# Kernel tuning notes

Hardware: AMD Instinct MI355X
Metric: run time of the kernel (lower is better)

Reference implementation:

```python
import jax, jax.numpy as jnp
import numpy as np

D_MODEL = 1024
NUM_HEADS = 16
D_K = D_MODEL // NUM_HEADS
ROPE_THETA = 10000.0


def setup_inputs() -> dict:
    key = jax.random.key(0)
    kx, kq, kk, kv, ko = jax.random.split(key, 5)
    B, S = 4, 2048
    std = (2.0 / (D_MODEL + D_MODEL)) ** 0.5
    def w(k):
        return jax.random.truncated_normal(k, -3.0, 3.0, (D_MODEL, D_MODEL), jnp.float32) * std
    return {
        "x": jax.random.normal(kx, (B, S, D_MODEL), jnp.float32),
        "Wq": w(kq), "Wk": w(kk), "Wv": w(kv), "Wo": w(ko),
    }


def _apply_rope(t):
    # t: [B, H, S, d_k]
    S, dk = t.shape[-2], t.shape[-1]
    inv_freq = 1.0 / (ROPE_THETA ** (jnp.arange(0, dk, 2) / dk))  # [dk/2]
    angles = jnp.outer(jnp.arange(S), inv_freq)                    # [S, dk/2]
    cos = jnp.repeat(jnp.cos(angles), 2, axis=-1).astype(t.dtype)  # [S, dk]
    sin = jnp.repeat(jnp.sin(angles), 2, axis=-1).astype(t.dtype)
    t_even = t[..., 0::2]
    t_odd = t[..., 1::2]
    t_rot = jnp.stack([-t_odd, t_even], axis=-1).reshape(t.shape)
    return t * cos + t_rot * sin


def reference(x, Wq, Wk, Wv, Wo):
    B, S, D = x.shape
    H, dk = NUM_HEADS, D_K
    q = jnp.einsum("bsi,io->bso", x, Wq).reshape(B, S, H, dk).swapaxes(1, 2)
    k = jnp.einsum("bsi,io->bso", x, Wk).reshape(B, S, H, dk).swapaxes(1, 2)
    v = jnp.einsum("bsi,io->bso", x, Wv).reshape(B, S, H, dk).swapaxes(1, 2)
    q = _apply_rope(q)
    k = _apply_rope(k)
    scores = jnp.einsum("bhqd,bhkd->bhqk", q, k) / (dk ** 0.5)  # [B,H,S,S]
    causal = jnp.tril(jnp.ones((S, S), dtype=bool))
    scores = jnp.where(causal, scores, -jnp.inf)
    attn = jax.nn.softmax(scores, axis=-1)
    out = jnp.einsum("bhqk,bhkd->bhqd", attn, v)  # [B,H,S,dk]
    out = out.swapaxes(1, 2).reshape(B, S, D)
    return jnp.einsum("bsi,io->bso", out, Wo)
```

## Files before the change

### kernel.cpp

```cpp
#include <hip/hip_runtime.h>
#include <hip/hip_bf16.h>

#define SEQ   2048
#define NB    4
#define NH    16
#define DK    64
#define DM    1024
#define MROWS (NB * SEQ)
#define WEL   (DM * DM)

typedef __bf16 bf16_t;
typedef __bf16 bf16x8 __attribute__((ext_vector_type(8)));
typedef __bf16 bf16x4 __attribute__((ext_vector_type(4)));
typedef float  f32x4  __attribute__((ext_vector_type(4)));

#define MFMA16(a, b, c) __builtin_amdgcn_mfma_f32_16x16x32_bf16((a), (b), (c), 0, 0, 0)

__device__ __forceinline__ void gl2lds16(const bf16_t* g, bf16_t* l) {
    __builtin_amdgcn_global_load_lds(
        (const __attribute__((address_space(1))) unsigned int*)g,
        (__attribute__((address_space(3))) unsigned int*)l, 16, 0, 0);
}

#define BAR()   __builtin_amdgcn_s_barrier()
#define SCB()   __builtin_amdgcn_sched_barrier(0)
#define LGK0()  asm volatile("s_waitcnt lgkmcnt(0)")
#define LGK8()  asm volatile("s_waitcnt lgkmcnt(8)")
#define VMC(N)  asm volatile("s_waitcnt vmcnt(" #N ")")

__global__ __launch_bounds__(256) void prep_kernel(
    const float* __restrict__ x,
    const float* __restrict__ Wq, const float* __restrict__ Wk,
    const float* __restrict__ Wv, const float* __restrict__ Wo,
    bf16_t* __restrict__ xb, bf16_t* __restrict__ Wqkvt,
    bf16_t* __restrict__ Wot, float2* __restrict__ rope)
{
    __shared__ float T[32][33];
    const int bid = blockIdx.x;
    const int tid = threadIdx.x;

    if (bid < 8192) {
        const int i = (bid * 256 + tid) * 4;
        const float4 v = *(const float4*)(x + i);
        bf16x4 o;
        o[0] = (bf16_t)v.x; o[1] = (bf16_t)v.y;
        o[2] = (bf16_t)v.z; o[3] = (bf16_t)v.w;
        *(bf16x4*)(xb + i) = o;
    } else if (bid < 12288) {
        const int wb = bid - 8192;
        const int w  = wb >> 10;
        const int b10 = wb & 1023;
        const float* W = (w == 0) ? Wq : (w == 1) ? Wk : (w == 2) ? Wv : Wo;
        bf16_t* Wt = (w == 3) ? Wot : Wqkvt + (size_t)w * WEL;
        const int tk0 = (b10 >> 5) << 5;
        const int tn0 = (b10 & 31) << 5;
        const int r = tid >> 5, c = tid & 31;
#pragma unroll
        for (int i = 0; i < 4; ++i)
            T[r + i * 8][c] = W[(size_t)(tk0 + r + i * 8) * DM + tn0 + c];
        __syncthreads();
#pragma unroll
        for (int i = 0; i < 4; ++i)
            Wt[(size_t)(tn0 + r + i * 8) * DM + tk0 + c] = (bf16_t)T[c][r + i * 8];
    } else {
        const int idx = (bid - 12288) * 256 + tid;
        const int s = idx >> 5, i = idx & 31;
        const float freq = powf(10000.0f, -(float)i / 32.0f);
        const float a = (float)s * freq;
        rope[idx] = make_float2(cosf(a), sinf(a));
    }
}

template<bool TR>
__device__ __forceinline__ void kloop(
    const bf16_t* __restrict__ Xp, const bf16_t* __restrict__ Wp,
    bf16_t* L, int tid, f32x4 (&acc)[8][4])
{
    const int lane = tid & 63;
    const int wave = tid >> 6;
    const int wm   = wave >> 2;
    const int wn   = wave & 3;
    const int lrow = lane & 15;
    const int lcol = (lane >> 4) << 3;

    bf16_t* const AR = L;
    bf16_t* const BR = L + 32768;

    const bf16_t* pA0 = Xp + (size_t)(wave * 16 + lrow) * DM + lcol;
    const bf16_t* pA1 = pA0 + (size_t)128 * DM;
    const bf16_t* pB0 = Wp + (size_t)(wave * 16 + lrow) * DM + lcol;
    const bf16_t* pB1 = pB0 + (size_t)128 * DM;

    bf16_t* const adst = AR + wave * 1024;
    bf16_t* const bdst = BR + wave * 1024;

    const bf16_t* const Ard = AR + wm * 8192;
    const bf16_t* const Brd = BR + wn * 4096;

    bf16x8 a[2][2], bc[4][2];

#define RD_A(BUF, Q)                                                          \
    a[0][0] = *(const bf16x8*)(Ard + (BUF) + (2*(Q)+0)*1024 + lane*8);        \
    a[0][1] = *(const bf16x8*)(Ard + (BUF) + (2*(Q)+0)*1024 + 512 + lane*8);  \
    a[1][0] = *(const bf16x8*)(Ard + (BUF) + (2*(Q)+1)*1024 + lane*8);        \
    a[1][1] = *(const bf16x8*)(Ard + (BUF) + (2*(Q)+1)*1024 + 512 + lane*8);

#define RD_B(BUF, NF)                                                         \
    bc[NF][0] = *(const bf16x8*)(Brd + (BUF) + (NF)*1024 + lane*8);           \
    bc[NF][1] = *(const bf16x8*)(Brd + (BUF) + (NF)*1024 + 512 + lane*8);

#define ST_A(BUF, H, C)                                                       \
    gl2lds16(((H) ? pA1 : pA0) + (C),      adst + (BUF) + (H)*8192);          \
    gl2lds16(((H) ? pA1 : pA0) + (C) + 32, adst + (BUF) + (H)*8192 + 512);

#define ST_B(BUF, H, C)                                                       \
    gl2lds16(((H) ? pB1 : pB0) + (C),      bdst + (BUF) + (H)*8192);          \
    gl2lds16(((H) ? pB1 : pB0) + (C) + 32, bdst + (BUF) + (H)*8192 + 512);

#define QMMA(Q)                                                               \
    __builtin_amdgcn_s_setprio(1);                                            \
    _Pragma("unroll")                                                         \
    for (int nf = 0; nf < 4; ++nf) {                                          \
        if (TR) {                                                             \
            acc[2*(Q)][nf]   = MFMA16(bc[nf][0], a[0][0], acc[2*(Q)][nf]);    \
            acc[2*(Q)][nf]   = MFMA16(bc[nf][1], a[0][1], acc[2*(Q)][nf]);    \
            acc[2*(Q)+1][nf] = MFMA16(bc[nf][0], a[1][0], acc[2*(Q)+1][nf]);  \
            acc[2*(Q)+1][nf] = MFMA16(bc[nf][1], a[1][1], acc[2*(Q)+1][nf]);  \
        } else {                                                              \
            acc[2*(Q)][nf]   = MFMA16(a[0][0], bc[nf][0], acc[2*(Q)][nf]);    \
            acc[2*(Q)][nf]   = MFMA16(a[0][1], bc[nf][1], acc[2*(Q)][nf]);    \
            acc[2*(Q)+1][nf] = MFMA16(a[1][0], bc[nf][0], acc[2*(Q)+1][nf]);  \
            acc[2*(Q)+1][nf] = MFMA16(a[1][1], bc[nf][1], acc[2*(Q)+1][nf]);  \
        }                                                                     \
    }                                                                         \
    __builtin_amdgcn_s_setprio(0);

    ST_B(0, 0, 0)      ST_B(0, 1, 0)
    ST_A(0, 0, 0)      ST_A(0, 1, 0)
    ST_B(16384, 0, 64) ST_B(16384, 1, 64)
    VMC(4);
    BAR();

    for (int it = 0; it < 8; ++it) {
        const bool lst = (it == 7);

        RD_A(0, 0) RD_B(0, 0) RD_B(0, 1) RD_B(0, 2) RD_B(0, 3)
        ST_A(16384, 0, 64) ST_A(16384, 1, 64)
        LGK8();
        BAR(); LGK0(); SCB();
        QMMA(0)
        BAR();

        RD_A(0, 1)
        if (!lst) { ST_B(0, 0, 128) }
        BAR(); LGK0(); SCB();
        QMMA(1)
        BAR();

        RD_A(0, 2)
        if (!lst) { ST_B(0, 1, 128) }
        BAR(); LGK0(); SCB();
        QMMA(2)
        BAR();

        RD_A(0, 3)
        BAR(); LGK0(); SCB();
        QMMA(3)
        if (lst) { VMC(0); } else { VMC(4); }
        BAR();

        RD_A(16384, 0) RD_B(16384, 0) RD_B(16384, 1) RD_B(16384, 2) RD_B(16384, 3)
        if (!lst) { ST_A(0, 0, 128) }
        LGK8();
        BAR(); LGK0(); SCB();
        QMMA(0)
        BAR();

        RD_A(16384, 1)
        if (!lst) { ST_A(0, 1, 128) }
        BAR(); LGK0(); SCB();
        QMMA(1)
        BAR();

        RD_A(16384, 2)
        if (!lst) { ST_B(16384, 0, 192) }
        BAR(); LGK0(); SCB();
        QMMA(2)
        BAR();

        RD_A(16384, 3)
        if (!lst) { ST_B(16384, 1, 192) }
        BAR(); LGK0(); SCB();
        QMMA(3)
        if (!lst) { VMC(4); }
        BAR();

        pA0 += 128; pA1 += 128; pB0 += 128; pB1 += 128;
    }

#undef QMMA
#undef ST_B
#undef ST_A
#undef RD_B
#undef RD_A
}

__global__ __launch_bounds__(512, 2) void gemm_qkv_kernel(
    const bf16_t* __restrict__ X, const bf16_t* __restrict__ Wt,
    bf16_t* __restrict__ Qt, bf16_t* __restrict__ Kt, bf16_t* __restrict__ Vtr,
    const float2* __restrict__ rope)
{
    __shared__ __align__(16) bf16_t L[65536];

    const int tid = threadIdx.x;
    const int xcd = blockIdx.x & 7;
    const int idx = blockIdx.x >> 3;
    const int mt  = xcd * 4 + (idx & 3);
    const int nt  = idx >> 2;
    const int m0 = mt << 8, n0 = nt << 8;
    const bool tr = (n0 >= 2 * DM);

    f32x4 acc[8][4] = {};
    if (tr) kloop<true >(X + (size_t)m0 * DM, Wt + (size_t)n0 * DM, L, tid, acc);
    else    kloop<false>(X + (size_t)m0 * DM, Wt + (size_t)n0 * DM, L, tid, acc);

    const int lane = tid & 63;
    const int wave = tid >> 6;
    const int wm   = wave >> 2, wn = wave & 3;
    const int l    = lane & 15;
    const int quad = lane >> 4;

#pragma unroll
    for (int mf = 0; mf < 8; ++mf)
#pragma unroll
        for (int nf = 0; nf < 4; ++nf)
#pragma unroll
            for (int r = 0; r < 4; ++r) {
                float v = acc[mf][nf][r];
                if (tr) {
                    const int n = n0 + wn * 64 + nf * 16 + quad * 4 + r;
                    const int m = m0 + wm * 128 + mf * 16 + l;
                    const int bi = m >> 11, s = m & (SEQ - 1);
                    const int col = n & (DM - 1);
                    const int h = col >> 6, d = col & (DK - 1);
                    Vtr[(((size_t)(bi * NH + h)) * DK + d) * SEQ + s] = (bf16_t)v;
                } else {
                    const int m  = m0 + wm * 128 + mf * 16 + quad * 4 + r;
                    const int nn = n0 + wn * 64 + nf * 16 + l;
                    const int bi = m >> 11, s = m & (SEQ - 1);
                    const int col = nn & (DM - 1);
                    const int h = col >> 6, d = col & (DK - 1);
                    float pv = __shfl_xor(v, 1);
                    float2 cs = rope[s * 32 + (d >> 1)];
                    float res = (d & 1) ? (v * cs.x + pv * cs.y)
                                        : (v * cs.x - pv * cs.y);
                    bf16_t* dst = (nn < DM) ? Qt : Kt;
                    if (nn < DM) res *= 0.125f;
                    dst[(((size_t)(bi * NH + h)) * SEQ + s) * DK + d] = (bf16_t)res;
                }
            }
}

__global__ __launch_bounds__(512, 2) void gemm_out_kernel(
    const bf16_t* __restrict__ X, const bf16_t* __restrict__ Wt,
    float* __restrict__ out)
{
    __shared__ __align__(16) bf16_t L[49152];

    const int tid = threadIdx.x;
    const int xcd = blockIdx.x & 7;
    const int idx = blockIdx.x >> 3;
    const int mt  = xcd * 8 + (idx & 7);
    const int nt  = idx >> 3;
    const int m0 = mt << 7, n0 = nt << 8;

    const int lane = tid & 63;
    const int wave = tid >> 6;
    const int wm   = wave >> 2;
    const int wn   = wave & 3;
    const int lrow = lane & 15;
    const int lcol = (lane >> 4) << 3;

    bf16_t* const AR = L;
    bf16_t* const BR = L + 16384;

    const bf16_t* Xp = X + (size_t)m0 * DM;
    const bf16_t* Wp = Wt + (size_t)n0 * DM;
    const bf16_t* pA  = Xp + (size_t)(wave * 16 + lrow) * DM + lcol;
    const bf16_t* pB0 = Wp + (size_t)(wave * 16 + lrow) * DM + lcol;
    const bf16_t* pB1 = pB0 + (size_t)128 * DM;

    bf16_t* const adst = AR + wave * 1024;
    bf16_t* const bdst = BR + wave * 1024;

    const bf16_t* const Ard = AR + wm * 4096;
    const bf16_t* const Brd = BR + wn * 4096;

    f32x4 acc[4][4] = {};
    bf16x8 a[2][2], bc[4][2];

#define RD_AH(BUF, Q)                                                         \
    a[0][0] = *(const bf16x8*)(Ard + (BUF) + (2*(Q)+0)*1024 + lane*8);        \
    a[0][1] = *(const bf16x8*)(Ard + (BUF) + (2*(Q)+0)*1024 + 512 + lane*8);  \
    a[1][0] = *(const bf16x8*)(Ard + (BUF) + (2*(Q)+1)*1024 + lane*8);        \
    a[1][1] = *(const bf16x8*)(Ard + (BUF) + (2*(Q)+1)*1024 + 512 + lane*8);

#define RD_BH(BUF, NF)                                                        \
    bc[NF][0] = *(const bf16x8*)(Brd + (BUF) + (NF)*1024 + lane*8);           \
    bc[NF][1] = *(const bf16x8*)(Brd + (BUF) + (NF)*1024 + 512 + lane*8);

#define ST_AH(BUF, C)                                                         \
    gl2lds16(pA + (C),      adst + (BUF));                                    \
    gl2lds16(pA + (C) + 32, adst + (BUF) + 512);

#define ST_BH(BUF, H, C)                                                      \
    gl2lds16(((H) ? pB1 : pB0) + (C),      bdst + (BUF) + (H)*8192);          \
    gl2lds16(((H) ? pB1 : pB0) + (C) + 32, bdst + (BUF) + (H)*8192 + 512);

#define QMMAH(Q)                                                              \
    __builtin_amdgcn_s_setprio(1);                                            \
    _Pragma("unroll")                                                         \
    for (int nf = 0; nf < 4; ++nf) {                                          \
        acc[2*(Q)][nf]   = MFMA16(a[0][0], bc[nf][0], acc[2*(Q)][nf]);        \
        acc[2*(Q)][nf]   = MFMA16(a[0][1], bc[nf][1], acc[2*(Q)][nf]);        \
        acc[2*(Q)+1][nf] = MFMA16(a[1][0], bc[nf][0], acc[2*(Q)+1][nf]);      \
        acc[2*(Q)+1][nf] = MFMA16(a[1][1], bc[nf][1], acc[2*(Q)+1][nf]);      \
    }                                                                         \
    __builtin_amdgcn_s_setprio(0);

    ST_AH(0, 0)
    ST_BH(0, 0, 0) ST_BH(0, 1, 0)
    ST_BH(16384, 0, 64) ST_BH(16384, 1, 64)
    VMC(4);
    BAR();

    for (int it = 0; it < 8; ++it) {
        const bool lst = (it == 7);

        RD_AH(0, 0) RD_BH(0, 0) RD_BH(0, 1) RD_BH(0, 2) RD_BH(0, 3)
        ST_AH(8192, 64)
        LGK8();
        BAR(); LGK0(); SCB();
        QMMAH(0)
        BAR();
        RD_AH(0, 1)
        if (!lst) { ST_BH(0, 0, 128) ST_BH(0, 1, 128) }
        BAR(); LGK0(); SCB();
        QMMAH(1)
        if (lst) { VMC(0); } else { VMC(4); }
        BAR();

        RD_AH(8192, 0) RD_BH(16384, 0) RD_BH(16384, 1) RD_BH(16384, 2) RD_BH(16384, 3)
        if (!lst) { ST_AH(0, 128) }
        LGK8();
        BAR(); LGK0(); SCB();
        QMMAH(0)
        BAR();
        RD_AH(8192, 1)
        if (!lst) { ST_BH(16384, 0, 192) ST_BH(16384, 1, 192) }
        BAR(); LGK0(); SCB();
        QMMAH(1)
        if (!lst) { VMC(4); }
        BAR();

        pA += 128; pB0 += 128; pB1 += 128;
    }

#undef QMMAH
#undef ST_BH
#undef ST_AH
#undef RD_BH
#undef RD_AH

    const int l    = lane & 15;
    const int quad = lane >> 4;
#pragma unroll
    for (int mf = 0; mf < 4; ++mf)
#pragma unroll
        for (int nf = 0; nf < 4; ++nf)
#pragma unroll
            for (int r = 0; r < 4; ++r) {
                const int m  = m0 + wm * 64 + mf * 16 + quad * 4 + r;
                const int nn = n0 + wn * 64 + nf * 16 + l;
                out[(size_t)m * DM + nn] = acc[mf][nf][r];
            }
}

#define KLD  72
#define KVSZ (64 * KLD)

__global__ __launch_bounds__(256) void attn_kernel(
    const bf16_t* __restrict__ Q, const bf16_t* __restrict__ K,
    const bf16_t* __restrict__ Vt, bf16_t* __restrict__ O)
{
    __shared__ __align__(16) bf16_t Kl[2 * KVSZ];
    __shared__ __align__(16) bf16_t Vl[2 * KVSZ];
    __shared__ __align__(16) bf16_t Pl[4][32 * KLD];

    const int bh   = blockIdx.x;
    const int qx   = blockIdx.y;
    const int tid  = threadIdx.x;
    const int wave = tid >> 6;
    const int lane = tid & 63;
    const int l    = lane & 15;
    const int quad = lane >> 4;
    const int srow = tid >> 3;
    const int sch  = (tid & 7) << 3;

    bf16_t* Pw = Pl[wave];
    const bf16_t* Qb = Q  + (size_t)bh * SEQ * DK;
    const bf16_t* Kb = K  + (size_t)bh * SEQ * DK;
    const bf16_t* Vb = Vt + (size_t)bh * DK * SEQ;
    const int b = bh >> 4, h = bh & 15;

    for (int ph = 0; ph < 2; ++ph) {
        const int qblk = ph ? (15 - qx) : qx;
        const int q0w  = qblk * 128 + wave * 32;
        const int nch  = 2 * (qblk + 1);

        bf16x8 qb[2][2];
#pragma unroll
        for (int u = 0; u < 2; ++u) {
            qb[u][0] = *(const bf16x8*)(Qb + (size_t)(q0w + u * 16 + l) * DK + quad * 8);
            qb[u][1] = *(const bf16x8*)(Qb + (size_t)(q0w + u * 16 + l) * DK + 32 + quad * 8);
        }

        float m_run[2] = {-3e38f, -3e38f};
        float l_run[2] = {0.f, 0.f};
        f32x4 o[4][2] = {};

        bf16x8 pk0 = *(const bf16x8*)(Kb + (size_t)srow * DK + sch);
        bf16x8 pk1 = *(const bf16x8*)(Kb + (size_t)(32 + srow) * DK + sch);
        bf16x8 pv0 = *(const bf16x8*)(Vb + (size_t)srow * SEQ + sch);
        bf16x8 pv1 = *(const bf16x8*)(Vb + (size_t)(32 + srow) * SEQ + sch);
        __syncthreads();
        *(bf16x8*)(Kl + srow * KLD + sch)        = pk0;
        *(bf16x8*)(Kl + (32 + srow) * KLD + sch) = pk1;
        *(bf16x8*)(Vl + srow * KLD + sch)        = pv0;
        *(bf16x8*)(Vl + (32 + srow) * KLD + sch) = pv1;
        __syncthreads();

        for (int i = 0; i < nch; ++i) {
            const int c  = i * 64;
            const int bf = (i & 1) * KVSZ;
            const int bn = ((i & 1) ^ 1) * KVSZ;
            const bool pf = (i + 1 < nch);

            if (pf) {
                const int cn = c + 64;
                pk0 = *(const bf16x8*)(Kb + (size_t)(cn + srow) * DK + sch);
                pk1 = *(const bf16x8*)(Kb + (size_t)(cn + 32 + srow) * DK + sch);
                pv0 = *(const bf16x8*)(Vb + (size_t)srow * SEQ + cn + sch);
                pv1 = *(const bf16x8*)(Vb + (size_t)(32 + srow) * SEQ + cn + sch);
            }

            if (c <= q0w + 31) {
                const bf16_t* Klb = Kl + bf;
                const bf16_t* Vlb = Vl + bf;

                f32x4 st[4][2] = {};
#pragma unroll
                for (int t = 0; t < 4; ++t) {
                    const bf16x8 k0 = *(const bf16x8*)(Klb + (t * 16 + l) * KLD + quad * 8);
                    const bf16x8 k1 = *(const bf16x8*)(Klb + (t * 16 + l) * KLD + 32 + quad * 8);
                    st[t][0] = MFMA16(k0, qb[0][0], st[t][0]);
                    st[t][0] = MFMA16(k1, qb[0][1], st[t][0]);
                    st[t][1] = MFMA16(k0, qb[1][0], st[t][1]);
                    st[t][1] = MFMA16(k1, qb[1][1], st[t][1]);
                }
                if (c + 63 > q0w) {
#pragma unroll
                    for (int u = 0; u < 2; ++u) {
                        const int thr = q0w + u * 16 + l - c - quad * 4;
#pragma unroll
                        for (int t = 0; t < 4; ++t)
#pragma unroll
                            for (int r = 0; r < 4; ++r)
                                if (t * 16 + r > thr) st[t][u][r] = -3e38f;
                    }
                }
#pragma unroll
                for (int u = 0; u < 2; ++u) {
                    float cmax = -3e38f;
#pragma unroll
                    for (int t = 0; t < 4; ++t)
#pragma unroll
                        for (int r = 0; r < 4; ++r)
                            cmax = fmaxf(cmax, st[t][u][r]);
                    cmax = fmaxf(cmax, __shfl_xor(cmax, 16));
                    cmax = fmaxf(cmax, __shfl_xor(cmax, 32));
                    const float mnew  = fmaxf(m_run[u], cmax);
                    const float alpha = __expf(m_run[u] - mnew);
                    m_run[u] = mnew;
                    float csum = 0.f;
#pragma unroll
                    for (int t = 0; t < 4; ++t)
#pragma unroll
                        for (int r = 0; r < 4; ++r) {
                            st[t][u][r] = __expf(st[t][u][r] - mnew);
                            csum += st[t][u][r];
                        }
                    csum += __shfl_xor(csum, 16);
                    csum += __shfl_xor(csum, 32);
                    l_run[u] = l_run[u] * alpha + csum;
#pragma unroll
                    for (int n = 0; n < 4; ++n)
#pragma unroll
                        for (int r = 0; r < 4; ++r)
                            o[n][u][r] *= alpha;
#pragma unroll
                    for (int t = 0; t < 4; ++t) {
                        bf16x4 pk;
                        pk[0] = (bf16_t)st[t][u][0]; pk[1] = (bf16_t)st[t][u][1];
                        pk[2] = (bf16_t)st[t][u][2]; pk[3] = (bf16_t)st[t][u][3];
                        *(bf16x4*)(Pw + (u * 16 + l) * KLD + t * 16 + quad * 4) = pk;
                    }
                }
                const bf16x8 pb00 = *(const bf16x8*)(Pw + l * KLD + quad * 8);
                const bf16x8 pb01 = *(const bf16x8*)(Pw + l * KLD + 32 + quad * 8);
                const bf16x8 pb10 = *(const bf16x8*)(Pw + (16 + l) * KLD + quad * 8);
                const bf16x8 pb11 = *(const bf16x8*)(Pw + (16 + l) * KLD + 32 + quad * 8);
#pragma unroll
                for (int n = 0; n < 4; ++n) {
                    const bf16x8 v0 = *(const bf16x8*)(Vlb + (n * 16 + l) * KLD + quad * 8);
                    const bf16x8 v1 = *(const bf16x8*)(Vlb + (n * 16 + l) * KLD + 32 + quad * 8);
                    o[n][0] = MFMA16(v0, pb00, o[n][0]);
                    o[n][0] = MFMA16(v1, pb01, o[n][0]);
                    o[n][1] = MFMA16(v0, pb10, o[n][1]);
                    o[n][1] = MFMA16(v1, pb11, o[n][1]);
                }
            }

            if (pf) {
                *(bf16x8*)(Kl + bn + srow * KLD + sch)        = pk0;
                *(bf16x8*)(Kl + bn + (32 + srow) * KLD + sch) = pk1;
                *(bf16x8*)(Vl + bn + srow * KLD + sch)        = pv0;
                *(bf16x8*)(Vl + bn + (32 + srow) * KLD + sch) = pv1;
            }
            __syncthreads();
        }

#pragma unroll
        for (int u = 0; u < 2; ++u) {
            const float inv = 1.0f / l_run[u];
#pragma unroll
            for (int n = 0; n < 4; ++n) {
                bf16x4 ov;
                ov[0] = (bf16_t)(o[n][u][0] * inv); ov[1] = (bf16_t)(o[n][u][1] * inv);
                ov[2] = (bf16_t)(o[n][u][2] * inv); ov[3] = (bf16_t)(o[n][u][3] * inv);
                *(bf16x4*)(Pw + (u * 16 + l) * KLD + n * 16 + quad * 4) = ov;
            }
        }
        const int row  = lane >> 1;
        const int half = (lane & 1) * 32;
        const bf16x8 w0 = *(const bf16x8*)(Pw + row * KLD + half);
        const bf16x8 w1 = *(const bf16x8*)(Pw + row * KLD + half + 8);
        const bf16x8 w2 = *(const bf16x8*)(Pw + row * KLD + half + 16);
        const bf16x8 w3 = *(const bf16x8*)(Pw + row * KLD + half + 24);
        bf16_t* op = O + ((size_t)(b * SEQ + qblk * 128 + wave * 32 + row)) * DM
                       + h * DK + half;
        *(bf16x8*)(op)      = w0;
        *(bf16x8*)(op + 8)  = w1;
        *(bf16x8*)(op + 16) = w2;
        *(bf16x8*)(op + 24) = w3;
    }
}

extern "C" void kernel_launch(void* const* d_in, const int* in_sizes, int n_in,
                              void* d_out, int out_size, void* d_ws, size_t ws_size,
                              hipStream_t stream)
{
    const float* x  = (const float*)d_in[0];
    const float* Wq = (const float*)d_in[1];
    const float* Wk = (const float*)d_in[2];
    const float* Wv = (const float*)d_in[3];
    const float* Wo = (const float*)d_in[4];

    char* ws = (char*)d_ws;
    float2* rope = (float2*)ws;
    const size_t TEN = (size_t)MROWS * DM;
    bf16_t* xb    = (bf16_t*)(ws + (1 << 19));
    bf16_t* Wqkvt = xb + TEN;
    bf16_t* Wot   = Wqkvt + 3 * (size_t)WEL;
    bf16_t* Qt    = Wot + WEL;
    bf16_t* Kt    = Qt + TEN;
    bf16_t* Vt    = Kt + TEN;
    bf16_t* Ot    = Vt + TEN;

    prep_kernel<<<12544, 256, 0, stream>>>(x, Wq, Wk, Wv, Wo,
                                           xb, Wqkvt, Wot, rope);

    gemm_qkv_kernel<<<32 * 12, 512, 0, stream>>>(xb, Wqkvt, Qt, Kt, Vt, rope);

    attn_kernel<<<dim3(NB * NH, 8), 256, 0, stream>>>(Qt, Kt, Vt, Ot);

    gemm_out_kernel<<<64 * 4, 512, 0, stream>>>(Ot, Wot, (float*)d_out);
}
```

Measured before the change: 299.3 us.

## Load K/V fragments directly from global in attention, drop LDS staging and barriers

Removes the shared-memory double buffer for K and V in the attention kernel. Each wave now reads its MFMA fragments straight from global memory, relying on L1/L2, and runs only as many key chunks as its own causal range needs. This eliminates the block-wide __syncthreads per chunk and lets waves proceed independently. It adds s_setprio around the MFMA sections. The trade-off is redundant global/L2 traffic across the four waves and exposed load latency, since nothing prefetches ahead.

```diff
diff --git a/kernel.cpp b/kernel.cpp
--- a/kernel.cpp
+++ b/kernel.cpp
@@ -386,15 +386,12 @@
             }
 }
 
-#define KLD  72
-#define KVSZ (64 * KLD)
+#define KLD 72
 
 __global__ __launch_bounds__(256) void attn_kernel(
     const bf16_t* __restrict__ Q, const bf16_t* __restrict__ K,
     const bf16_t* __restrict__ Vt, bf16_t* __restrict__ O)
 {
-    __shared__ __align__(16) bf16_t Kl[2 * KVSZ];
-    __shared__ __align__(16) bf16_t Vl[2 * KVSZ];
     __shared__ __align__(16) bf16_t Pl[4][32 * KLD];
 
     const int bh   = blockIdx.x;
@@ -404,8 +401,6 @@
     const int lane = tid & 63;
     const int l    = lane & 15;
     const int quad = lane >> 4;
-    const int srow = tid >> 3;
-    const int sch  = (tid & 7) << 3;
 
     bf16_t* Pw = Pl[wave];
     const bf16_t* Qb = Q  + (size_t)bh * SEQ * DK;
@@ -416,7 +411,7 @@
     for (int ph = 0; ph < 2; ++ph) {
         const int qblk = ph ? (15 - qx) : qx;
         const int q0w  = qblk * 128 + wave * 32;
-        const int nch  = 2 * (qblk + 1);
+        const int nchw = 2 * qblk + 1 + (wave >> 1);
 
         bf16x8 qb[2][2];
 #pragma unroll
@@ -429,115 +424,92 @@
         float l_run[2] = {0.f, 0.f};
         f32x4 o[4][2] = {};
 
-        bf16x8 pk0 = *(const bf16x8*)(Kb + (size_t)srow * DK + sch);
-        bf16x8 pk1 = *(const bf16x8*)(Kb + (size_t)(32 + srow) * DK + sch);
-        bf16x8 pv0 = *(const bf16x8*)(Vb + (size_t)srow * SEQ + sch);
-        bf16x8 pv1 = *(const bf16x8*)(Vb + (size_t)(32 + srow) * SEQ + sch);
-        __syncthreads();
-        *(bf16x8*)(Kl + srow * KLD + sch)        = pk0;
-        *(bf16x8*)(Kl + (32 + srow) * KLD + sch) = pk1;
-        *(bf16x8*)(Vl + srow * KLD + sch)        = pv0;
-        *(bf16x8*)(Vl + (32 + srow) * KLD + sch) = pv1;
-        __syncthreads();
-
-        for (int i = 0; i < nch; ++i) {
-            const int c  = i * 64;
-            const int bf = (i & 1) * KVSZ;
-            const int bn = ((i & 1) ^ 1) * KVSZ;
-            const bool pf = (i + 1 < nch);
-
-            if (pf) {
-                const int cn = c + 64;
-                pk0 = *(const bf16x8*)(Kb + (size_t)(cn + srow) * DK + sch);
-                pk1 = *(const bf16x8*)(Kb + (size_t)(cn + 32 + srow) * DK + sch);
-                pv0 = *(const bf16x8*)(Vb + (size_t)srow * SEQ + cn + sch);
-                pv1 = *(const bf16x8*)(Vb + (size_t)(32 + srow) * SEQ + cn + sch);
-            }
-
-            if (c <= q0w + 31) {
-                const bf16_t* Klb = Kl + bf;
-                const bf16_t* Vlb = Vl + bf;
-
-                f32x4 st[4][2] = {};
+        for (int i = 0; i < nchw; ++i) {
+            const int c = i * 64;
+
+            f32x4 st[4][2] = {};
+            __builtin_amdgcn_s_setprio(1);
+#pragma unroll
+            for (int t = 0; t < 4; ++t) {
+                const bf16x8 k0 = *(const bf16x8*)(Kb + (size_t)(c + t * 16 + l) * DK + quad * 8);
+                const bf16x8 k1 = *(const bf16x8*)(Kb + (size_t)(c + t * 16 + l) * DK + 32 + quad * 8);
+                st[t][0] = MFMA16(k0, qb[0][0], st[t][0]);
+                st[t][0] = MFMA16(k1, qb[0][1], st[t][0]);
+                st[t][1] = MFMA16(k0, qb[1][0], st[t][1]);
+                st[t][1] = MFMA16(k1, qb[1][1], st[t][1]);
+            }
+            __builtin_amdgcn_s_setprio(0);
+
+            bf16x8 vf[4][2];
+#pragma unroll
+            for (int n = 0; n < 4; ++n) {
+                vf[n][0] = *(const bf16x8*)(Vb + (size_t)(n * 16 + l) * SEQ + c + quad * 8);
+                vf[n][1] = *(const bf16x8*)(Vb + (size_t)(n * 16 + l) * SEQ + c + 32 + quad * 8);
+            }
+
+            if (c + 63 > q0w) {
+#pragma unroll
+                for (int u = 0; u < 2; ++u) {
+                    const int thr = q0w + u * 16 + l - c - quad * 4;
+#pragma unroll
+                    for (int t = 0; t < 4; ++t)
+#pragma unroll
+                        for (int r = 0; r < 4; ++r)
+                            if (t * 16 + r > thr) st[t][u][r] = -3e38f;
+                }
+            }
+
+#pragma unroll
+            for (int u = 0; u < 2; ++u) {
+                float cmax = -3e38f;
+#pragma unroll
+                for (int t = 0; t < 4; ++t)
+#pragma unroll
+                    for (int r = 0; r < 4; ++r)
+                        cmax = fmaxf(cmax, st[t][u][r]);
+                cmax = fmaxf(cmax, __shfl_xor(cmax, 16));
+                cmax = fmaxf(cmax, __shfl_xor(cmax, 32));
+                const float mnew  = fmaxf(m_run[u], cmax);
+                const float alpha = __expf(m_run[u] - mnew);
+                m_run[u] = mnew;
+                float csum = 0.f;
+#pragma unroll
+                for (int t = 0; t < 4; ++t)
+#pragma unroll
+                    for (int r = 0; r < 4; ++r) {
+                        st[t][u][r] = __expf(st[t][u][r] - mnew);
+                        csum += st[t][u][r];
+                    }
+                csum += __shfl_xor(csum, 16);
+                csum += __shfl_xor(csum, 32);
+                l_run[u] = l_run[u] * alpha + csum;
+#pragma unroll
+                for (int n = 0; n < 4; ++n)
+#pragma unroll
+                    for (int r = 0; r < 4; ++r)
+                        o[n][u][r] *= alpha;
 #pragma unroll
                 for (int t = 0; t < 4; ++t) {
-                    const bf16x8 k0 = *(const bf16x8*)(Klb + (t * 16 + l) * KLD + quad * 8);
-                    const bf16x8 k1 = *(const bf16x8*)(Klb + (t * 16 + l) * KLD + 32 + quad * 8);
-                    st[t][0] = MFMA16(k0, qb[0][0], st[t][0]);
-                    st[t][0] = MFMA16(k1, qb[0][1], st[t][0]);
-                    st[t][1] = MFMA16(k0, qb[1][0], st[t][1]);
-                    st[t][1] = MFMA16(k1, qb[1][1], st[t][1]);
+                    bf16x4 pk;
+                    pk[0] = (bf16_t)st[t][u][0]; pk[1] = (bf16_t)st[t][u][1];
+                    pk[2] = (bf16_t)st[t][u][2]; pk[3] = (bf16_t)st[t][u][3];
+                    *(bf16x4*)(Pw + (u * 16 + l) * KLD + t * 16 + quad * 4) = pk;
                 }
-                if (c + 63 > q0w) {
-#pragma unroll
-                    for (int u = 0; u < 2; ++u) {
-                        const int thr = q0w + u * 16 + l - c - quad * 4;
-#pragma unroll
-                        for (int t = 0; t < 4; ++t)
-#pragma unroll
-                            for (int r = 0; r < 4; ++r)
-                                if (t * 16 + r > thr) st[t][u][r] = -3e38f;
-                    }
-                }
-#pragma unroll
-                for (int u = 0; u < 2; ++u) {
-                    float cmax = -3e38f;
-#pragma unroll
-                    for (int t = 0; t < 4; ++t)
-#pragma unroll
-                        for (int r = 0; r < 4; ++r)
-                            cmax = fmaxf(cmax, st[t][u][r]);
-                    cmax = fmaxf(cmax, __shfl_xor(cmax, 16));
-                    cmax = fmaxf(cmax, __shfl_xor(cmax, 32));
-                    const float mnew  = fmaxf(m_run[u], cmax);
-                    const float alpha = __expf(m_run[u] - mnew);
-                    m_run[u] = mnew;
-                    float csum = 0.f;
-#pragma unroll
-                    for (int t = 0; t < 4; ++t)
-#pragma unroll
-                        for (int r = 0; r < 4; ++r) {
-                            st[t][u][r] = __expf(st[t][u][r] - mnew);
-                            csum += st[t][u][r];
-                        }
-                    csum += __shfl_xor(csum, 16);
-                    csum += __shfl_xor(csum, 32);
-                    l_run[u] = l_run[u] * alpha + csum;
-#pragma unroll
-                    for (int n = 0; n < 4; ++n)
-#pragma unroll
-                        for (int r = 0; r < 4; ++r)
-                            o[n][u][r] *= alpha;
-#pragma unroll
-                    for (int t = 0; t < 4; ++t) {
-                        bf16x4 pk;
-                        pk[0] = (bf16_t)st[t][u][0]; pk[1] = (bf16_t)st[t][u][1];
-                        pk[2] = (bf16_t)st[t][u][2]; pk[3] = (bf16_t)st[t][u][3];
-                        *(bf16x4*)(Pw + (u * 16 + l) * KLD + t * 16 + quad * 4) = pk;
-                    }
-                }
-                const bf16x8 pb00 = *(const bf16x8*)(Pw + l * KLD + quad * 8);
-                const bf16x8 pb01 = *(const bf16x8*)(Pw + l * KLD + 32 + quad * 8);
-                const bf16x8 pb10 = *(const bf16x8*)(Pw + (16 + l) * KLD + quad * 8);
-                const bf16x8 pb11 = *(const bf16x8*)(Pw + (16 + l) * KLD + 32 + quad * 8);
-#pragma unroll
-                for (int n = 0; n < 4; ++n) {
-                    const bf16x8 v0 = *(const bf16x8*)(Vlb + (n * 16 + l) * KLD + quad * 8);
-                    const bf16x8 v1 = *(const bf16x8*)(Vlb + (n * 16 + l) * KLD + 32 + quad * 8);
-                    o[n][0] = MFMA16(v0, pb00, o[n][0]);
-                    o[n][0] = MFMA16(v1, pb01, o[n][0]);
-                    o[n][1] = MFMA16(v0, pb10, o[n][1]);
-                    o[n][1] = MFMA16(v1, pb11, o[n][1]);
-                }
-            }
-
-            if (pf) {
-                *(bf16x8*)(Kl + bn + srow * KLD + sch)        = pk0;
-                *(bf16x8*)(Kl + bn + (32 + srow) * KLD + sch) = pk1;
-                *(bf16x8*)(Vl + bn + srow * KLD + sch)        = pv0;
-                *(bf16x8*)(Vl + bn + (32 + srow) * KLD + sch) = pv1;
-            }
-            __syncthreads();
+            }
+
+            const bf16x8 pb00 = *(const bf16x8*)(Pw + l * KLD + quad * 8);
+            const bf16x8 pb01 = *(const bf16x8*)(Pw + l * KLD + 32 + quad * 8);
+            const bf16x8 pb10 = *(const bf16x8*)(Pw + (16 + l) * KLD + quad * 8);
+            const bf16x8 pb11 = *(const bf16x8*)(Pw + (16 + l) * KLD + 32 + quad * 8);
+            __builtin_amdgcn_s_setprio(1);
+#pragma unroll
+            for (int n = 0; n < 4; ++n) {
+                o[n][0] = MFMA16(vf[n][0], pb00, o[n][0]);
+                o[n][0] = MFMA16(vf[n][1], pb01, o[n][0]);
+                o[n][1] = MFMA16(vf[n][0], pb10, o[n][1]);
+                o[n][1] = MFMA16(vf[n][1], pb11, o[n][1]);
+            }
+            __builtin_amdgcn_s_setprio(0);
         }
 
 #pragma unroll
```

Measured after the change: 345.0 us. 1.15x slower.
